# Performance work log

Measured on AMD Instinct MI355X. Metric: run time of the kernel, lower is better.

The kernel has to match this reference:

```python
import jax, jax.numpy as jnp
import numpy as np

SIZE = 128
DELTA = 1.0
NUM_SHELLS = SIZE // 2  # 64 shells up to Nyquist; corners beyond Nyquist are discarded
DROP_DC = False
ALPHA = None
EPS = 1e-8


def _make_shell_idx(n, delta):
    # integer-frequency radial coordinate, same grid as torch.fft.fftfreq(n)*n
    f = np.fft.fftfreq(n) * n
    fx, fy, fz = np.meshgrid(f, f, f, indexing="ij")
    r = np.sqrt(fx * fx + fy * fy + fz * fz)
    idx = np.floor(r / delta).astype(np.int32)
    # voxels past the Nyquist shell go to a discard bucket (index NUM_SHELLS)
    idx = np.where(idx < NUM_SHELLS, idx, NUM_SHELLS)
    return idx


def setup_inputs() -> dict:
    key = jax.random.key(0)
    k1, k2 = jax.random.split(key)
    shape = (8, 1, SIZE, SIZE, SIZE)
    img_ref = jax.random.normal(k1, shape, dtype=jnp.float32)
    img_pred = jax.random.normal(k2, shape, dtype=jnp.float32)
    shell_idx = jnp.asarray(_make_shell_idx(SIZE, DELTA))
    return {"img_ref": img_ref, "img_pred": img_pred, "shell_idx": shell_idx}


def reference(img_ref, img_pred, shell_idx):
    B = img_ref.shape[0] * img_ref.shape[1]
    V = SIZE * SIZE * SIZE
    F1 = jnp.fft.fftn(img_ref, axes=(-3, -2, -1)).reshape(B, V)
    F2 = jnp.fft.fftn(img_pred, axes=(-3, -2, -1)).reshape(B, V)
    idx = shell_idx.reshape(V)

    # per-shell reductions (single pass, replaces num_shells dense mask-multiplies)
    cross = (F1 * jnp.conj(F2)).real          # Re sum F1 conj(F2) per shell
    p1 = (F1.real ** 2 + F1.imag ** 2)
    p2 = (F2.real ** 2 + F2.imag ** 2)

    seg = jax.vmap(lambda x: jax.ops.segment_sum(x, idx, num_segments=NUM_SHELLS + 1))
    num = seg(cross)[:, :NUM_SHELLS]          # [B, num_shells], drop discard bucket
    d1 = seg(p1)[:, :NUM_SHELLS]
    d2 = seg(p2)[:, :NUM_SHELLS]

    fsc = num / (jnp.sqrt(d1 * d2) + EPS)     # [B, num_shells]

    if ALPHA is not None:
        freq = (jnp.arange(NUM_SHELLS, dtype=jnp.float32) + 0.5) * DELTA / SIZE
        fsc = fsc * (freq ** ALPHA)
    if DROP_DC:
        fsc = fsc[:, 1:]

    loss = 1.0 - jnp.mean(fsc ** 2)
    return loss
```

## Files before the change

kernel.cpp:

```cpp
#include <hip/hip_runtime.h>
#include <math.h>

#define N      128
#define NSQ    (N * N)
#define VOL    (N * N * N)
#define NSHELL 64
#define BTOT   8
#define FPI    3.14159265358979323846f

#define TPX    17

__device__ inline void mk_tw(int l, float* tc, float* ts) {
    __sincosf(-FPI * (float)l * (1.0f / 64.0f), &ts[0], &tc[0]);
#pragma unroll
    for (int k = 1; k <= 6; ++k) {
        const int h = 64 >> k;
        float s, c;
        __sincosf(-FPI * (float)(l & (h - 1)) / (float)h, &s, &c);
        const bool hi = (l & h) != 0;
        tc[k] = hi ? c : 1.0f;
        ts[k] = hi ? s : 0.0f;
    }
}

__device__ inline void fft128(float2& v0, float2& v1,
                              const float* tc, const float* ts, int l) {
    {
        const float dx = v0.x - v1.x, dy = v0.y - v1.y;
        v0.x += v1.x; v0.y += v1.y;
        v1.x = dx * tc[0] - dy * ts[0];
        v1.y = dx * ts[0] + dy * tc[0];
    }
#pragma unroll
    for (int k = 1; k <= 6; ++k) {
        const int h = 64 >> k;
        const float e = (l & h) ? -1.0f : 1.0f;
        const float c = tc[k], s = ts[k];
        const float o0x = __shfl_xor(v0.x, h), o0y = __shfl_xor(v0.y, h);
        const float o1x = __shfl_xor(v1.x, h), o1y = __shfl_xor(v1.y, h);
        const float t0x = fmaf(e, v0.x, o0x), t0y = fmaf(e, v0.y, o0y);
        const float t1x = fmaf(e, v1.x, o1x), t1y = fmaf(e, v1.y, o1y);
        v0.x = t0x * c - t0y * s;  v0.y = t0x * s + t0y * c;
        v1.x = t1x * c - t1y * s;  v1.y = t1x * s + t1y * c;
    }
}

__device__ inline int binof(int s) {
    return (int)(((__brev((unsigned)(s >> 1)) >> 26) << 1) | (unsigned)(s & 1));
}

__global__ __launch_bounds__(1024) void k_fft_zy(const float* __restrict__ ref,
                                                 const float* __restrict__ pred,
                                                 float2* __restrict__ Z, int b0) {
    __shared__ float2 P0[64 * 128];
    __shared__ float2 P1[64 * 128];
    const int t = threadIdx.x, l = t & 63, w = t >> 6;
    const int x  = blockIdx.x & (N - 1);
    const int bl = blockIdx.x >> 7;
    float tc[7], ts[7];
    mk_tw(l, tc, ts);
    const int f2 = (int)(__brev((unsigned)l) >> 26) << 1;

    const size_t inb = (size_t)(b0 + bl) * VOL + (size_t)x * NSQ;
    const float* rp = ref  + inb;
    const float* pq = pred + inb;

    float2 V0[8], V1[8];
#pragma unroll
    for (int k = 0; k < 8; ++k) {
        const int y = w * 8 + k;
        V0[k] = make_float2(rp[y * N + l],      pq[y * N + l]);
        V1[k] = make_float2(rp[y * N + l + 64], pq[y * N + l + 64]);
    }
#pragma unroll
    for (int k = 0; k < 8; ++k) fft128(V0[k], V1[k], tc, ts, l);
    const int row = l * 128, sw = l & 31;
#pragma unroll
    for (int k = 0; k < 8; ++k) {
        const int c = (w * 8 + k) ^ sw;
        P0[row + c] = V0[k];
        P1[row + c] = V1[k];
    }
    __syncthreads();

    float2 U0[8], U1[8];
#pragma unroll
    for (int k = 0; k < 8; ++k) {
        const int s = w * 8 + k, j = s >> 1;
        const float2* PP = (s & 1) ? P1 : P0;
        const int c = l ^ (j & 31);
        U0[k] = PP[j * 128 + c];
        U1[k] = PP[j * 128 + c + 64];
    }
#pragma unroll
    for (int k = 0; k < 8; ++k) fft128(U0[k], U1[k], tc, ts, l);
    const size_t zb = (size_t)bl * VOL + (size_t)x * NSQ;
#pragma unroll
    for (int k = 0; k < 8; ++k) {
        const int s = w * 8 + k;
        *reinterpret_cast<float4*>(&Z[zb + (size_t)s * N + f2]) =
            make_float4(U0[k].x, U0[k].y, U1[k].x, U1[k].y);
    }
}

__device__ inline int isqrt_i(int r2) {
    int s = (int)sqrtf((float)r2);
    s -= (s * s > r2);
    s += ((s + 1) * (s + 1) <= r2);
    return s;
}

__global__ __launch_bounds__(512) void k_fftx_reduce(const float2* __restrict__ Z,
                                                     float* __restrict__ accum, int b0) {
    const int t = threadIdx.x, l = t & 63, w = t >> 6;
    const int yc = blockIdx.x & 7;
    const int q  = (blockIdx.x >> 3) & 63;
    const int bl = blockIdx.x >> 9;

    const int zs  = ((q >> 1) << 2) | (q & 1);
    const int fz  = binof(zs);
    const int fzz = fz * fz;
    const int minfy = (yc < 4) ? yc * 16 : 113 - yc * 16;
    if (fzz + minfy * minfy >= NSHELL * NSHELL) return;

    __shared__ float reA[128 * TPX], imA[128 * TPX];
    __shared__ float reB[128 * TPX], imB[128 * TPX];
    __shared__ float bins[4 * 193];

    const int mzs = binof((N - fz) & (N - 1));
    const int y0  = yc * 16;
    const size_t zbase = (size_t)bl * VOL;
#pragma unroll
    for (int qq = 0; qq < 4; ++qq) {
        const int e  = qq * 512 + t;
        const int xx = e >> 4, yi = e & 15;
        const int y  = y0 + yi;
        const int my = (N - y) & (N - 1);
        const float2 av = Z[zbase + (size_t)xx * NSQ + (size_t)zs  * N + y];
        const float2 bv = Z[zbase + (size_t)xx * NSQ + (size_t)mzs * N + my];
        reA[xx * TPX + yi] = av.x; imA[xx * TPX + yi] = av.y;
        reB[xx * TPX + yi] = bv.x; imB[xx * TPX + yi] = bv.y;
    }
    for (int i = t; i < 4 * 193; i += 512) bins[i] = 0.f;

    float tc[7], ts[7];
    mk_tw(l, tc, ts);
    const int B6 = (int)(__brev((unsigned)l) >> 26);
    const int f2 = B6 << 1;
    const int p0 = (int)(__brev((unsigned)((64 - B6) & 63)) >> 26);
    const int p1 = 63 - l;
    const int fx0 = f2 - ((f2 >= 64) ? N : 0);
    const int fx0s = fx0 * fx0;
    const int fx1s = (fx0 + 1) * (fx0 + 1);
    __syncthreads();

    const int yv0 = y0 + w * 2;
    const int fy0 = yv0 - ((yv0 >= 64) ? N : 0);
    const int fy1 = (yv0 + 1) - (((yv0 + 1) >= 64) ? N : 0);
    const int r2yz[2] = { fy0 * fy0 + fzz, fy1 * fy1 + fzz };
    float* mybins = bins + (t & 3) * 193;

#define FLUSH(CS, C, P1V, P2V)                                                \
    if ((unsigned)(CS) < (unsigned)NSHELL) {                                  \
        atomicAdd(&mybins[(CS) * 3 + 0], (C));                                \
        atomicAdd(&mybins[(CS) * 3 + 1], (P1V));                              \
        atomicAdd(&mybins[(CS) * 3 + 2], (P2V));                              \
    }
    if (r2yz[0] < NSHELL * NSHELL || r2yz[1] < NSHELL * NSHELL) {
        float2 A0[2], A1[2], M0[2], M1[2];
#pragma unroll
        for (int k = 0; k < 2; ++k) {
            const int yi = w * 2 + k;
            A0[k] = make_float2(reA[l * TPX + yi],        imA[l * TPX + yi]);
            A1[k] = make_float2(reA[(l + 64) * TPX + yi], imA[(l + 64) * TPX + yi]);
            M0[k] = make_float2(reB[l * TPX + yi],        imB[l * TPX + yi]);
            M1[k] = make_float2(reB[(l + 64) * TPX + yi], imB[(l + 64) * TPX + yi]);
        }
#pragma unroll
        for (int k = 0; k < 2; ++k) {
            fft128(A0[k], A1[k], tc, ts, l);
            fft128(M0[k], M1[k], tc, ts, l);
        }
        float rC0 = 0.f, rP10 = 0.f, rP20 = 0.f; int cs0 = -1;
        float rC1 = 0.f, rP11 = 0.f, rP21 = 0.f; int cs1 = -1;
#pragma unroll
        for (int k = 0; k < 2; ++k) {
            const float Bx0 = __shfl(M0[k].x, p0), By0 = __shfl(M0[k].y, p0);
            const float Bx1 = __shfl(M1[k].x, p1), By1 = __shfl(M1[k].y, p1);
            const int s0 = isqrt_i(fx0s + r2yz[k]);
            if (s0 != cs0) { FLUSH(cs0, rC0, rP10, rP20); cs0 = s0; rC0 = rP10 = rP20 = 0.f; }
            if (s0 < NSHELL) {
                const float F1x = 0.5f * (A0[k].x + Bx0);
                const float F1y = 0.5f * (A0[k].y - By0);
                const float F2x = 0.5f * (A0[k].y + By0);
                const float F2y = 0.5f * (Bx0 - A0[k].x);
                rC0  += F1x * F2x + F1y * F2y;
                rP10 += F1x * F1x + F1y * F1y;
                rP20 += F2x * F2x + F2y * F2y;
            }
            const int s1 = isqrt_i(fx1s + r2yz[k]);
            if (s1 != cs1) { FLUSH(cs1, rC1, rP11, rP21); cs1 = s1; rC1 = rP11 = rP21 = 0.f; }
            if (s1 < NSHELL) {
                const float F1x = 0.5f * (A1[k].x + Bx1);
                const float F1y = 0.5f * (A1[k].y - By1);
                const float F2x = 0.5f * (A1[k].y + By1);
                const float F2y = 0.5f * (Bx1 - A1[k].x);
                rC1  += F1x * F2x + F1y * F2y;
                rP11 += F1x * F1x + F1y * F1y;
                rP21 += F2x * F2x + F2y * F2y;
            }
        }
        FLUSH(cs0, rC0, rP10, rP20);
        FLUSH(cs1, rC1, rP11, rP21);
    }
#undef FLUSH
    __syncthreads();

    const float wsc = (fz == 0) ? 1.f : 2.f;
    const int smin = isqrt_i(fzz + minfy * minfy);
    float* acc = accum + (size_t)(b0 + bl) * (NSHELL * 3);
    for (int i = smin * 3 + t; i < NSHELL * 3; i += 512) {
        const float v = bins[i] + bins[193 + i] + bins[2 * 193 + i] + bins[3 * 193 + i];
        atomicAdd(&acc[i], v * wsc);
    }
}

__global__ __launch_bounds__(512) void k_final(const float* __restrict__ accum,
                                               float* __restrict__ out) {
    __shared__ float red[8];
    const int tid = threadIdx.x;
    const float* a = accum + (size_t)tid * 3;
    const float fsc = a[0] / (sqrtf(a[1] * a[2]) + 1e-8f);
    float v = fsc * fsc;
#pragma unroll
    for (int off = 32; off > 0; off >>= 1) v += __shfl_down(v, off);
    if ((tid & 63) == 0) red[tid >> 6] = v;
    __syncthreads();
    if (tid == 0) {
        float ssum = 0.f;
#pragma unroll
        for (int i = 0; i < 8; ++i) ssum += red[i];
        out[0] = 1.0f - ssum / 512.0f;
    }
}

extern "C" void kernel_launch(void* const* d_in, const int* in_sizes, int n_in,
                              void* d_out, int out_size, void* d_ws, size_t ws_size,
                              hipStream_t stream) {
    const float* ref  = (const float*)d_in[0];
    const float* pred = (const float*)d_in[1];
    float* out = (float*)d_out;

    char*   ws    = (char*)d_ws;
    float*  accum = (float*)ws;
    float2* Zbuf  = (float2*)(ws + 8192);

    const size_t zbytes = (size_t)VOL * sizeof(float2);
    int cap = 1;
    if (ws_size > 8192) {
        size_t c = (ws_size - 8192) / zbytes;
        cap = (c < 1) ? 1 : (c > BTOT ? BTOT : (int)c);
    }

    hipMemsetAsync(accum, 0, BTOT * NSHELL * 3 * sizeof(float), stream);

    for (int b0 = 0; b0 < BTOT; b0 += cap) {
        const int nb = (BTOT - b0 < cap) ? (BTOT - b0) : cap;
        k_fft_zy<<<nb * 128, 1024, 0, stream>>>(ref, pred, Zbuf, b0);
        k_fftx_reduce<<<nb * 512, 512, 0, stream>>>(Zbuf, accum, b0);
    }
    k_final<<<1, 512, 0, stream>>>(accum, out);
}
```

Before: 337.8 us.

## Replace ds_bpermute shuffles in FFT butterflies with DPP, swizzle and permlane swaps

Rewrites the 128-point wavefront FFT so that cross-lane exchanges use the cheapest available primitive at each stride. Strides 1, 2 and 8 use DPP row ops and stride 4 uses ds_swizzle. Strides 32 and 16 use permlane32/16 swap when the builtin exists, processing two FFTs jointly so each swap exchanges useful data. The last stage drops the trivial twiddle multiply. This targets the LDS-routed shfl_xor cost that dominates the butterfly stages. The price is more register pressure and reliance on the permlane builtins being available, with a plain shfl fallback otherwise.

```diff
diff --git a/kernel.cpp b/kernel.cpp
--- a/kernel.cpp
+++ b/kernel.cpp
@@ -10,39 +10,142 @@
 
 #define TPX    17
 
-__device__ inline void mk_tw(int l, float* tc, float* ts) {
-    __sincosf(-FPI * (float)l * (1.0f / 64.0f), &ts[0], &tc[0]);
-#pragma unroll
-    for (int k = 1; k <= 6; ++k) {
-        const int h = 64 >> k;
-        float s, c;
-        __sincosf(-FPI * (float)(l & (h - 1)) / (float)h, &s, &c);
-        const bool hi = (l & h) != 0;
-        tc[k] = hi ? c : 1.0f;
-        ts[k] = hi ? s : 0.0f;
-    }
-}
-
-__device__ inline void fft128(float2& v0, float2& v1,
-                              const float* tc, const float* ts, int l) {
-    {
-        const float dx = v0.x - v1.x, dy = v0.y - v1.y;
-        v0.x += v1.x; v0.y += v1.y;
-        v1.x = dx * tc[0] - dy * ts[0];
-        v1.y = dx * ts[0] + dy * tc[0];
-    }
-#pragma unroll
-    for (int k = 1; k <= 6; ++k) {
-        const int h = 64 >> k;
-        const float e = (l & h) ? -1.0f : 1.0f;
-        const float c = tc[k], s = ts[k];
-        const float o0x = __shfl_xor(v0.x, h), o0y = __shfl_xor(v0.y, h);
-        const float o1x = __shfl_xor(v1.x, h), o1y = __shfl_xor(v1.y, h);
-        const float t0x = fmaf(e, v0.x, o0x), t0y = fmaf(e, v0.y, o0y);
-        const float t1x = fmaf(e, v1.x, o1x), t1y = fmaf(e, v1.y, o1y);
-        v0.x = t0x * c - t0y * s;  v0.y = t0x * s + t0y * c;
-        v1.x = t1x * c - t1y * s;  v1.y = t1x * s + t1y * c;
-    }
+#if __has_builtin(__builtin_amdgcn_permlane32_swap) && __has_builtin(__builtin_amdgcn_permlane16_swap)
+#define HAVE_PLSWAP 1
+#else
+#define HAVE_PLSWAP 0
+#endif
+
+typedef unsigned uint2v __attribute__((ext_vector_type(2)));
+
+struct TW {
+    float c64, s64;
+    float c32, s32, c16, s16;
+#if !HAVE_PLSWAP
+    float e32, e16;
+#endif
+    float c8, s8, e8;
+    float c4, s4, e4;
+    float c2, s2, e2;
+    float e1;
+};
+
+__device__ inline void mk_tw(int l, TW& w) {
+    __sincosf(-FPI * (float)l * (1.0f / 64.0f), &w.s64, &w.c64);
+#if HAVE_PLSWAP
+    __sincosf(-FPI * (float)(l & 31) * (1.0f / 32.0f), &w.s32, &w.c32);
+    __sincosf(-FPI * (float)(l & 15) * (1.0f / 16.0f), &w.s16, &w.c16);
+#else
+    { float s, c; __sincosf(-FPI * (float)(l & 31) * (1.0f / 32.0f), &s, &c);
+      const bool hi = (l & 32); w.c32 = hi ? c : 1.f; w.s32 = hi ? s : 0.f; w.e32 = hi ? -1.f : 1.f; }
+    { float s, c; __sincosf(-FPI * (float)(l & 15) * (1.0f / 16.0f), &s, &c);
+      const bool hi = (l & 16); w.c16 = hi ? c : 1.f; w.s16 = hi ? s : 0.f; w.e16 = hi ? -1.f : 1.f; }
+#endif
+    { float s, c; __sincosf(-FPI * (float)(l & 7) * (1.0f / 8.0f), &s, &c);
+      const bool hi = (l & 8); w.c8 = hi ? c : 1.f; w.s8 = hi ? s : 0.f; w.e8 = hi ? -1.f : 1.f; }
+    { float s, c; __sincosf(-FPI * (float)(l & 3) * (1.0f / 4.0f), &s, &c);
+      const bool hi = (l & 4); w.c4 = hi ? c : 1.f; w.s4 = hi ? s : 0.f; w.e4 = hi ? -1.f : 1.f; }
+    { float s, c; __sincosf(-FPI * (float)(l & 1) * (1.0f / 2.0f), &s, &c);
+      const bool hi = (l & 2); w.c2 = hi ? c : 1.f; w.s2 = hi ? s : 0.f; w.e2 = hi ? -1.f : 1.f; }
+    w.e1 = (l & 1) ? -1.f : 1.f;
+}
+
+template<int CTRL>
+__device__ inline float2 xdpp(float2 v) {
+    return make_float2(
+        __int_as_float(__builtin_amdgcn_update_dpp(__float_as_int(v.x), __float_as_int(v.x), CTRL, 0xF, 0xF, false)),
+        __int_as_float(__builtin_amdgcn_update_dpp(__float_as_int(v.y), __float_as_int(v.y), CTRL, 0xF, 0xF, false)));
+}
+__device__ inline float2 xswz4(float2 v) {
+    return make_float2(
+        __int_as_float(__builtin_amdgcn_ds_swizzle(__float_as_int(v.x), 0x101F)),
+        __int_as_float(__builtin_amdgcn_ds_swizzle(__float_as_int(v.y), 0x101F)));
+}
+
+__device__ inline float2 bfly(float2 v, float2 o, float c, float s, float e) {
+    const float tx = fmaf(e, v.x, o.x), ty = fmaf(e, v.y, o.y);
+    return make_float2(tx * c - ty * s, tx * s + ty * c);
+}
+
+__device__ inline void bf64(float2& v0, float2& v1, float c, float s) {
+    const float dx = v0.x - v1.x, dy = v0.y - v1.y;
+    v0.x += v1.x; v0.y += v1.y;
+    v1.x = dx * c - dy * s;
+    v1.y = dx * s + dy * c;
+}
+
+#if HAVE_PLSWAP
+__device__ inline void swp32f(float& a, float& b) {
+    uint2v r = __builtin_amdgcn_permlane32_swap(__float_as_uint(a), __float_as_uint(b), false, false);
+    a = __uint_as_float(r[0]); b = __uint_as_float(r[1]);
+}
+__device__ inline void swp16f(float& a, float& b) {
+    uint2v r = __builtin_amdgcn_permlane16_swap(__float_as_uint(a), __float_as_uint(b), false, false);
+    a = __uint_as_float(r[0]); b = __uint_as_float(r[1]);
+}
+__device__ inline void pair32(float2& A, float2& B, float c, float s) {
+    float P = A.x, Q = B.x, R = A.y, S = B.y;
+    swp32f(P, Q); swp32f(R, S);
+    const float sx = P + Q, sy = R + S;
+    const float dx = P - Q, dy = R - S;
+    float fx = dx * c - dy * s;
+    float fy = dx * s + dy * c;
+    float ax = sx, bx = fx, ay = sy, by = fy;
+    swp32f(ax, bx); swp32f(ay, by);
+    A = make_float2(ax, ay); B = make_float2(bx, by);
+}
+__device__ inline void pair16(float2& A, float2& B, float c, float s) {
+    float P = A.x, Q = B.x, R = A.y, S = B.y;
+    swp16f(P, Q); swp16f(R, S);
+    const float sx = P + Q, sy = R + S;
+    const float dx = P - Q, dy = R - S;
+    float fx = dx * c - dy * s;
+    float fy = dx * s + dy * c;
+    float ax = sx, bx = fx, ay = sy, by = fy;
+    swp16f(ax, bx); swp16f(ay, by);
+    A = make_float2(ax, ay); B = make_float2(bx, by);
+}
+#else
+__device__ inline float2 xshfl(float2 v, int m) {
+    return make_float2(__shfl_xor(v.x, m), __shfl_xor(v.y, m));
+}
+#endif
+
+__device__ inline void fft128p(float2& a0, float2& a1, float2& b0, float2& b1,
+                               const TW& w) {
+    bf64(a0, a1, w.c64, w.s64);
+    bf64(b0, b1, w.c64, w.s64);
+#if HAVE_PLSWAP
+    pair32(a0, b0, w.c32, w.s32);
+    pair32(a1, b1, w.c32, w.s32);
+    pair16(a0, b0, w.c16, w.s16);
+    pair16(a1, b1, w.c16, w.s16);
+#else
+    { float2 o = xshfl(a0, 32); a0 = bfly(a0, o, w.c32, w.s32, w.e32); }
+    { float2 o = xshfl(a1, 32); a1 = bfly(a1, o, w.c32, w.s32, w.e32); }
+    { float2 o = xshfl(b0, 32); b0 = bfly(b0, o, w.c32, w.s32, w.e32); }
+    { float2 o = xshfl(b1, 32); b1 = bfly(b1, o, w.c32, w.s32, w.e32); }
+    { float2 o = xshfl(a0, 16); a0 = bfly(a0, o, w.c16, w.s16, w.e16); }
+    { float2 o = xshfl(a1, 16); a1 = bfly(a1, o, w.c16, w.s16, w.e16); }
+    { float2 o = xshfl(b0, 16); b0 = bfly(b0, o, w.c16, w.s16, w.e16); }
+    { float2 o = xshfl(b1, 16); b1 = bfly(b1, o, w.c16, w.s16, w.e16); }
+#endif
+    { float2 o = xdpp<0x128>(a0); a0 = bfly(a0, o, w.c8, w.s8, w.e8); }
+    { float2 o = xdpp<0x128>(a1); a1 = bfly(a1, o, w.c8, w.s8, w.e8); }
+    { float2 o = xdpp<0x128>(b0); b0 = bfly(b0, o, w.c8, w.s8, w.e8); }
+    { float2 o = xdpp<0x128>(b1); b1 = bfly(b1, o, w.c8, w.s8, w.e8); }
+    { float2 o = xswz4(a0); a0 = bfly(a0, o, w.c4, w.s4, w.e4); }
+    { float2 o = xswz4(a1); a1 = bfly(a1, o, w.c4, w.s4, w.e4); }
+    { float2 o = xswz4(b0); b0 = bfly(b0, o, w.c4, w.s4, w.e4); }
+    { float2 o = xswz4(b1); b1 = bfly(b1, o, w.c4, w.s4, w.e4); }
+    { float2 o = xdpp<0x4E>(a0); a0 = bfly(a0, o, w.c2, w.s2, w.e2); }
+    { float2 o = xdpp<0x4E>(a1); a1 = bfly(a1, o, w.c2, w.s2, w.e2); }
+    { float2 o = xdpp<0x4E>(b0); b0 = bfly(b0, o, w.c2, w.s2, w.e2); }
+    { float2 o = xdpp<0x4E>(b1); b1 = bfly(b1, o, w.c2, w.s2, w.e2); }
+    { float2 o = xdpp<0xB1>(a0); a0.x = fmaf(w.e1, a0.x, o.x); a0.y = fmaf(w.e1, a0.y, o.y); }
+    { float2 o = xdpp<0xB1>(a1); a1.x = fmaf(w.e1, a1.x, o.x); a1.y = fmaf(w.e1, a1.y, o.y); }
+    { float2 o = xdpp<0xB1>(b0); b0.x = fmaf(w.e1, b0.x, o.x); b0.y = fmaf(w.e1, b0.y, o.y); }
+    { float2 o = xdpp<0xB1>(b1); b1.x = fmaf(w.e1, b1.x, o.x); b1.y = fmaf(w.e1, b1.y, o.y); }
 }
 
 __device__ inline int binof(int s) {
@@ -57,8 +160,8 @@
     const int t = threadIdx.x, l = t & 63, w = t >> 6;
     const int x  = blockIdx.x & (N - 1);
     const int bl = blockIdx.x >> 7;
-    float tc[7], ts[7];
-    mk_tw(l, tc, ts);
+    TW tw;
+    mk_tw(l, tw);
     const int f2 = (int)(__brev((unsigned)l) >> 26) << 1;
 
     const size_t inb = (size_t)(b0 + bl) * VOL + (size_t)x * NSQ;
@@ -73,7 +176,8 @@
         V1[k] = make_float2(rp[y * N + l + 64], pq[y * N + l + 64]);
     }
 #pragma unroll
-    for (int k = 0; k < 8; ++k) fft128(V0[k], V1[k], tc, ts, l);
+    for (int k = 0; k < 8; k += 2)
+        fft128p(V0[k], V1[k], V0[k + 1], V1[k + 1], tw);
     const int row = l * 128, sw = l & 31;
 #pragma unroll
     for (int k = 0; k < 8; ++k) {
@@ -93,7 +197,8 @@
         U1[k] = PP[j * 128 + c + 64];
     }
 #pragma unroll
-    for (int k = 0; k < 8; ++k) fft128(U0[k], U1[k], tc, ts, l);
+    for (int k = 0; k < 8; k += 2)
+        fft128p(U0[k], U1[k], U0[k + 1], U1[k + 1], tw);
     const size_t zb = (size_t)bl * VOL + (size_t)x * NSQ;
 #pragma unroll
     for (int k = 0; k < 8; ++k) {
@@ -143,8 +248,8 @@
     }
     for (int i = t; i < 4 * 193; i += 512) bins[i] = 0.f;
 
-    float tc[7], ts[7];
-    mk_tw(l, tc, ts);
+    TW tw;
+    mk_tw(l, tw);
     const int B6 = (int)(__brev((unsigned)l) >> 26);
     const int f2 = B6 << 1;
     const int p0 = (int)(__brev((unsigned)((64 - B6) & 63)) >> 26);
@@ -176,11 +281,8 @@
             M0[k] = make_float2(reB[l * TPX + yi],        imB[l * TPX + yi]);
             M1[k] = make_float2(reB[(l + 64) * TPX + yi], imB[(l + 64) * TPX + yi]);
         }
-#pragma unroll
-        for (int k = 0; k < 2; ++k) {
-            fft128(A0[k], A1[k], tc, ts, l);
-            fft128(M0[k], M1[k], tc, ts, l);
-        }
+        fft128p(A0[0], A1[0], A0[1], A1[1], tw);
+        fft128p(M0[0], M1[0], M0[1], M1[1], tw);
         float rC0 = 0.f, rP10 = 0.f, rP20 = 0.f; int cs0 = -1;
         float rC1 = 0.f, rP11 = 0.f, rP21 = 0.f; int cs1 = -1;
 #pragma unroll
```

Result: faster. 292.7 us (-13.3%).
